# Performance work log

Measured on AMD Instinct MI355X. Metric: run time of the kernel, lower is better.

## Reference

```python
import jax, jax.numpy as jnp
import numpy as np

NUM_EXPERTS = 8
HIDDEN = 1024
INTER = 1024
TOKENS = 2048
TOPK = 2


def setup_inputs() -> dict:
    key = jax.random.key(0)
    ks = jax.random.split(key, 7)
    hidden_states = jax.random.normal(ks[0], (TOKENS, HIDDEN), dtype=jnp.float32)
    router_weights = jax.random.uniform(ks[1], (TOKENS, TOPK), dtype=jnp.float32)
    selected_experts = jax.random.randint(ks[2], (TOKENS, TOPK), 0, NUM_EXPERTS, dtype=jnp.int32)
    token_per_expert = jax.random.randint(ks[3], (NUM_EXPERTS,), 0, 512, dtype=jnp.int32)
    # torch Linear weight layout is [out, in]; chunked along out-dim into E experts.
    # gate/up: [E, INTER, HIDDEN]; down: [E, HIDDEN, INTER]
    scale_h = 1.0 / np.sqrt(HIDDEN)
    scale_i = 1.0 / np.sqrt(INTER)
    gate_w = jax.random.normal(ks[4], (NUM_EXPERTS, INTER, HIDDEN), dtype=jnp.float32) * scale_h
    up_w = jax.random.normal(ks[5], (NUM_EXPERTS, INTER, HIDDEN), dtype=jnp.float32) * scale_h
    down_w = jax.random.normal(ks[6], (NUM_EXPERTS, HIDDEN, INTER), dtype=jnp.float32) * scale_i
    return {
        "hidden_states": hidden_states,
        "router_weights": router_weights,
        "selected_experts": selected_experts,
        "token_per_expert": token_per_expert,
        "gate_w": gate_w,
        "up_w": up_w,
        "down_w": down_w,
    }


def reference(hidden_states, router_weights, selected_experts, token_per_expert, gate_w, up_w, down_w):
    # Math equivalent of permute -> grouped GEMM (gate/up SwiGLU, down) -> unpermute+weighted combine.
    # Each (token, k) pair is routed to expert selected_experts[t,k] and scaled by router_weights[t,k]
    # (cast to fp32 as in the original), then summed over k.
    # Grouped GEMM out = x @ W_e^T; we evaluate every expert densely over all tokens and
    # combine with a one-hot routing matrix (clean, fully vectorized reference).
    x = hidden_states  # [T, H]
    g = jnp.einsum('th,eih->eti', x, gate_w)          # [E, T, I]
    u = jnp.einsum('th,eih->eti', x, up_w)            # [E, T, I]
    h = jax.nn.silu(g) * u                            # [E, T, I]
    out_e = jnp.einsum('eti,ehi->eth', h, down_w)     # [E, T, H]
    # combine[t, e] = sum_k router_weights[t, k] * 1[selected_experts[t, k] == e]
    onehot = jax.nn.one_hot(selected_experts, NUM_EXPERTS, dtype=jnp.float32)  # [T, K, E]
    combine = jnp.einsum('tk,tke->te', router_weights.astype(jnp.float32), onehot)  # [T, E]
    y = jnp.einsum('te,eth->th', combine, out_e)      # [T, H]
    return y
```

## Files before the change

### kernel.cpp

```cpp
#include <hip/hip_runtime.h>

#define T_TOK 2048
#define HID   1024
#define INTER_ 1024
#define NEXP  8
#define NPAIR 4096
#define PERM_MAX 4608

typedef unsigned short u16;
typedef __attribute__((ext_vector_type(8))) short bf16x8;
typedef __attribute__((ext_vector_type(4))) float f32x4;
typedef __attribute__((ext_vector_type(4))) unsigned short us4;
typedef __attribute__((ext_vector_type(4))) unsigned int u32x4;

static __device__ __forceinline__ u16 f2bf(float f) {
  union { float f; unsigned u; } v; v.f = f;
  unsigned u = v.u;
  unsigned r = (u + 0x7fffu + ((u >> 16) & 1u)) >> 16;
  return (u16)r;
}

__global__ __launch_bounds__(256) void k_prep(const float* __restrict__ x,
                                              u16* __restrict__ xb,
                                              float* __restrict__ out) {
  int i = blockIdx.x * 256 + threadIdx.x;
  int base = i * 8;
  f32x4 v0 = *(const f32x4*)(x + base);
  f32x4 v1 = *(const f32x4*)(x + base + 4);
  us4 a = { f2bf(v0[0]), f2bf(v0[1]), f2bf(v0[2]), f2bf(v0[3]) };
  us4 b = { f2bf(v1[0]), f2bf(v1[1]), f2bf(v1[2]), f2bf(v1[3]) };
  *(us4*)(xb + base)     = a;
  *(us4*)(xb + base + 4) = b;
  f32x4 z = {0.f, 0.f, 0.f, 0.f};
  *(f32x4*)(out + base)     = z;
  *(f32x4*)(out + base + 4) = z;
}

__global__ __launch_bounds__(256) void k_route(const int* __restrict__ sel,
                                               int* __restrict__ hdr,
                                               int* __restrict__ perm) {
  __shared__ int cnt[NEXP];
  __shared__ int cur[NEXP];
  int tid = threadIdx.x;
  if (tid < NEXP) cnt[tid] = 0;
  __syncthreads();
  for (int p = tid; p < NPAIR; p += 256) atomicAdd(&cnt[sel[p]], 1);
  __syncthreads();
  if (tid == 0) {
    int acc = 0;
    for (int e = 0; e < NEXP; e++) {
      hdr[e] = acc;
      cur[e] = acc;
      acc += (cnt[e] + 63) & ~63;
    }
    hdr[NEXP] = acc;
  }
  __syncthreads();
  for (int i = tid; i < PERM_MAX; i += 256) perm[i] = -1;
  __syncthreads();
  for (int p = tid; p < NPAIR; p += 256) {
    int e = sel[p];
    int slot = atomicAdd(&cur[e], 1);
    perm[slot] = p;
  }
}

__global__ __launch_bounds__(256) void k_gateup(const u16* __restrict__ xb,
                                                const float* __restrict__ gw,
                                                const float* __restrict__ uw,
                                                const int* __restrict__ hdr,
                                                const int* __restrict__ perm,
                                                u16* __restrict__ hbuf) {
  __shared__ __align__(16) u16 lA[4096];
  __shared__ __align__(16) u16 lBg[4096];
  __shared__ __align__(16) u16 lBu[4096];

  const int tid = threadIdx.x;
  const int lane = tid & 63;
  const int wv = tid >> 6;
  const int n0 = blockIdx.x * 64;
  const int m0 = blockIdx.y * 64;
  const int total = hdr[NEXP];
  if (m0 >= total) return;
  int e = 0;
  #pragma unroll
  for (int k = 1; k < NEXP; k++) if (m0 >= hdr[k]) e = k;

  const int c0 = tid, c1 = 256 + tid;
  const int r0 = c0 >> 3, q0 = c0 & 7;
  const int r1 = c1 >> 3, q1 = c1 & 7;
  const int p0 = perm[m0 + r0]; const int tok0 = (p0 < 0) ? 0 : (p0 >> 1);
  const int p1 = perm[m0 + r1]; const int tok1 = (p1 < 0) ? 0 : (p1 >> 1);
  const u16* gA0 = xb + (size_t)tok0 * HID + q0 * 8;
  const u16* gA1 = xb + (size_t)tok1 * HID + q1 * 8;
  const int lA0 = r0 * 64 + (q0 ^ (r0 & 7)) * 8;
  const int lA1 = r1 * 64 + (q1 ^ (r1 & 7)) * 8;

  const float* gB[4]; const float* gU[4]; int lB[4];
  const size_t ebase = (size_t)e * (size_t)(INTER_ * HID);
  #pragma unroll
  for (int i = 0; i < 4; i++) {
    int c = tid + 256 * i;
    int r = c >> 4, q4 = c & 15;
    gB[i] = gw + ebase + (size_t)(n0 + r) * HID + q4 * 4;
    gU[i] = uw + ebase + (size_t)(n0 + r) * HID + q4 * 4;
    lB[i] = r * 64 + (((q4 >> 1) ^ (r & 7)) * 8) + (q4 & 1) * 4;
  }

  const int wm = wv >> 1, wn = wv & 1;
  const int fr = lane & 15, fq = lane >> 4;

  f32x4 accg[2][2], accu[2][2];
  #pragma unroll
  for (int a = 0; a < 2; a++)
    #pragma unroll
    for (int b = 0; b < 2; b++) {
      accg[a][b] = (f32x4){0.f, 0.f, 0.f, 0.f};
      accu[a][b] = (f32x4){0.f, 0.f, 0.f, 0.f};
    }

  for (int kk = 0; kk < HID / 64; kk++) {
    const int k0 = kk * 64;
    *(u32x4*)&lA[lA0] = *(const u32x4*)(gA0 + k0);
    *(u32x4*)&lA[lA1] = *(const u32x4*)(gA1 + k0);
    #pragma unroll
    for (int i = 0; i < 4; i++) {
      f32x4 vg = *(const f32x4*)(gB[i] + k0);
      f32x4 vu = *(const f32x4*)(gU[i] + k0);
      us4 wg = { f2bf(vg[0]), f2bf(vg[1]), f2bf(vg[2]), f2bf(vg[3]) };
      us4 wu = { f2bf(vu[0]), f2bf(vu[1]), f2bf(vu[2]), f2bf(vu[3]) };
      *(us4*)&lBg[lB[i]] = wg;
      *(us4*)&lBu[lB[i]] = wu;
    }
    __syncthreads();
    #pragma unroll
    for (int kk2 = 0; kk2 < 2; kk2++) {
      bf16x8 af[2], bgf[2], buf_[2];
      #pragma unroll
      for (int m2 = 0; m2 < 2; m2++) {
        int r = wm * 32 + m2 * 16 + fr;
        int q = kk2 * 4 + fq;
        af[m2] = *(const bf16x8*)&lA[r * 64 + (q ^ (r & 7)) * 8];
      }
      #pragma unroll
      for (int n2 = 0; n2 < 2; n2++) {
        int r = wn * 32 + n2 * 16 + fr;
        int q = kk2 * 4 + fq;
        bgf[n2]  = *(const bf16x8*)&lBg[r * 64 + (q ^ (r & 7)) * 8];
        buf_[n2] = *(const bf16x8*)&lBu[r * 64 + (q ^ (r & 7)) * 8];
      }
      #pragma unroll
      for (int m2 = 0; m2 < 2; m2++)
        #pragma unroll
        for (int n2 = 0; n2 < 2; n2++) {
          accg[m2][n2] = __builtin_amdgcn_mfma_f32_16x16x32_bf16(af[m2], bgf[n2],  accg[m2][n2], 0, 0, 0);
          accu[m2][n2] = __builtin_amdgcn_mfma_f32_16x16x32_bf16(af[m2], buf_[n2], accu[m2][n2], 0, 0, 0);
        }
    }
    __syncthreads();
  }

  #pragma unroll
  for (int m2 = 0; m2 < 2; m2++)
    #pragma unroll
    for (int n2 = 0; n2 < 2; n2++)
      #pragma unroll
      for (int q = 0; q < 4; q++) {
        int row = m0 + wm * 32 + m2 * 16 + fq * 4 + q;
        int col = n0 + wn * 32 + n2 * 16 + fr;
        float g = accg[m2][n2][q];
        float u = accu[m2][n2][q];
        float h = (g / (1.0f + __expf(-g))) * u;
        hbuf[(size_t)row * INTER_ + col] = f2bf(h);
      }
}

__global__ __launch_bounds__(256) void k_down(const u16* __restrict__ hbuf,
                                              const float* __restrict__ dw,
                                              const int* __restrict__ hdr,
                                              const int* __restrict__ perm,
                                              const float* __restrict__ rw,
                                              float* __restrict__ out) {
  __shared__ __align__(16) u16 lA[4096];
  __shared__ __align__(16) u16 lB[4096];

  const int tid = threadIdx.x;
  const int lane = tid & 63;
  const int wv = tid >> 6;
  const int n0 = blockIdx.x * 64;
  const int m0 = blockIdx.y * 64;
  const int total = hdr[NEXP];
  if (m0 >= total) return;
  int e = 0;
  #pragma unroll
  for (int k = 1; k < NEXP; k++) if (m0 >= hdr[k]) e = k;

  const int c0 = tid, c1 = 256 + tid;
  const int r0 = c0 >> 3, q0 = c0 & 7;
  const int r1 = c1 >> 3, q1 = c1 & 7;
  const u16* gA0 = hbuf + (size_t)(m0 + r0) * INTER_ + q0 * 8;
  const u16* gA1 = hbuf + (size_t)(m0 + r1) * INTER_ + q1 * 8;
  const int lA0 = r0 * 64 + (q0 ^ (r0 & 7)) * 8;
  const int lA1 = r1 * 64 + (q1 ^ (r1 & 7)) * 8;

  const float* gB[4]; int lBo[4];
  const size_t ebase = (size_t)e * (size_t)(HID * INTER_);
  #pragma unroll
  for (int i = 0; i < 4; i++) {
    int c = tid + 256 * i;
    int r = c >> 4, q4 = c & 15;
    gB[i] = dw + ebase + (size_t)(n0 + r) * INTER_ + q4 * 4;
    lBo[i] = r * 64 + (((q4 >> 1) ^ (r & 7)) * 8) + (q4 & 1) * 4;
  }

  const int wm = wv >> 1, wn = wv & 1;
  const int fr = lane & 15, fq = lane >> 4;

  f32x4 acc[2][2];
  #pragma unroll
  for (int a = 0; a < 2; a++)
    #pragma unroll
    for (int b = 0; b < 2; b++) acc[a][b] = (f32x4){0.f, 0.f, 0.f, 0.f};

  for (int kk = 0; kk < INTER_ / 64; kk++) {
    const int k0 = kk * 64;
    *(u32x4*)&lA[lA0] = *(const u32x4*)(gA0 + k0);
    *(u32x4*)&lA[lA1] = *(const u32x4*)(gA1 + k0);
    #pragma unroll
    for (int i = 0; i < 4; i++) {
      f32x4 vb = *(const f32x4*)(gB[i] + k0);
      us4 wb = { f2bf(vb[0]), f2bf(vb[1]), f2bf(vb[2]), f2bf(vb[3]) };
      *(us4*)&lB[lBo[i]] = wb;
    }
    __syncthreads();
    #pragma unroll
    for (int kk2 = 0; kk2 < 2; kk2++) {
      bf16x8 af[2], bf[2];
      #pragma unroll
      for (int m2 = 0; m2 < 2; m2++) {
        int r = wm * 32 + m2 * 16 + fr;
        int q = kk2 * 4 + fq;
        af[m2] = *(const bf16x8*)&lA[r * 64 + (q ^ (r & 7)) * 8];
      }
      #pragma unroll
      for (int n2 = 0; n2 < 2; n2++) {
        int r = wn * 32 + n2 * 16 + fr;
        int q = kk2 * 4 + fq;
        bf[n2] = *(const bf16x8*)&lB[r * 64 + (q ^ (r & 7)) * 8];
      }
      #pragma unroll
      for (int m2 = 0; m2 < 2; m2++)
        #pragma unroll
        for (int n2 = 0; n2 < 2; n2++)
          acc[m2][n2] = __builtin_amdgcn_mfma_f32_16x16x32_bf16(af[m2], bf[n2], acc[m2][n2], 0, 0, 0);
    }
    __syncthreads();
  }

  #pragma unroll
  for (int m2 = 0; m2 < 2; m2++)
    #pragma unroll
    for (int q = 0; q < 4; q++) {
      int row = m0 + wm * 32 + m2 * 16 + fq * 4 + q;
      int p = perm[row];
      if (p < 0) continue;
      int t = p >> 1;
      float w = rw[p];
      #pragma unroll
      for (int n2 = 0; n2 < 2; n2++) {
        int col = n0 + wn * 32 + n2 * 16 + fr;
        atomicAdd(&out[(size_t)t * HID + col], acc[m2][n2][q] * w);
      }
    }
}

extern "C" void kernel_launch(void* const* d_in, const int* in_sizes, int n_in,
                              void* d_out, int out_size, void* d_ws, size_t ws_size,
                              hipStream_t stream) {
  const float* x   = (const float*)d_in[0];
  const float* rw  = (const float*)d_in[1];
  const int*   sel = (const int*)d_in[2];
  const float* gw  = (const float*)d_in[4];
  const float* uw  = (const float*)d_in[5];
  const float* dw  = (const float*)d_in[6];
  float* out = (float*)d_out;

  char* ws = (char*)d_ws;
  int*  hdr  = (int*)ws;
  int*  perm = (int*)(ws + 1024);
  u16*  xb   = (u16*)(ws + 32768);
  u16*  hbuf = (u16*)(ws + 32768 + 4 * 1024 * 1024);

  k_prep<<<dim3(1024), dim3(256), 0, stream>>>(x, xb, out);
  k_route<<<dim3(1), dim3(256), 0, stream>>>(sel, hdr, perm);
  k_gateup<<<dim3(16, 72), dim3(256), 0, stream>>>(xb, gw, uw, hdr, perm, hbuf);
  k_down<<<dim3(16, 72), dim3(256), 0, stream>>>(hbuf, dw, hdr, perm, rw, out);
}
```

Measured before the change: 101.7 us.

## Pre-convert expert weights to bf16, use direct global-to-LDS loads, 128-row tiles

Adds a separate kernel that converts all gate, up and down weights from fp32 to bf16 once per call. This replaces the per-tile fp32 load and conversion inside each GEMM block, which was repeated by every M-tile. The GEMM kernels now stage A and B tiles with global_load_lds 16-byte transfers and swizzled source addresses. The M tile grows to 128 rows, with expert segments padded to 128, so each weight tile is reused across more tokens. The trade-off is one extra full pass over the 96 MB of fp32 weights plus a bf16 write each call, and more padding rows per expert.

```diff
diff --git a/kernel.cpp b/kernel.cpp
--- a/kernel.cpp
+++ b/kernel.cpp
@@ -1,23 +1,32 @@
 #include <hip/hip_runtime.h>
 
-#define T_TOK 2048
 #define HID   1024
-#define INTER_ 1024
 #define NEXP  8
 #define NPAIR 4096
-#define PERM_MAX 4608
+#define BMPAD 128
+#define PERM_MAX (NPAIR + NEXP * BMPAD)
+#define MT_MAX (PERM_MAX / 128)
 
 typedef unsigned short u16;
 typedef __attribute__((ext_vector_type(8))) short bf16x8;
 typedef __attribute__((ext_vector_type(4))) float f32x4;
 typedef __attribute__((ext_vector_type(4))) unsigned short us4;
-typedef __attribute__((ext_vector_type(4))) unsigned int u32x4;
 
 static __device__ __forceinline__ u16 f2bf(float f) {
   union { float f; unsigned u; } v; v.f = f;
   unsigned u = v.u;
   unsigned r = (u + 0x7fffu + ((u >> 16) & 1u)) >> 16;
   return (u16)r;
+}
+
+static __device__ __forceinline__ void gload16(const void* g, void* l) {
+  __builtin_amdgcn_global_load_lds(
+      (const __attribute__((address_space(1))) unsigned int*)g,
+      (__attribute__((address_space(3))) unsigned int*)l, 16, 0, 0);
+}
+
+static __device__ __forceinline__ f32x4 mfma_bf16(bf16x8 a, bf16x8 b, f32x4 c) {
+  return __builtin_amdgcn_mfma_f32_16x16x32_bf16(a, b, c, 0, 0, 0);
 }
 
 __global__ __launch_bounds__(256) void k_prep(const float* __restrict__ x,
@@ -34,6 +43,27 @@
   f32x4 z = {0.f, 0.f, 0.f, 0.f};
   *(f32x4*)(out + base)     = z;
   *(f32x4*)(out + base + 4) = z;
+}
+
+__global__ __launch_bounds__(256) void k_convw(const float* __restrict__ g,
+                                               const float* __restrict__ u,
+                                               const float* __restrict__ d,
+                                               u16* __restrict__ gb,
+                                               u16* __restrict__ ub,
+                                               u16* __restrict__ db) {
+  const long NTH = 3L << 20;
+  for (long i = (long)blockIdx.x * 256 + threadIdx.x; i < NTH; i += (long)gridDim.x * 256) {
+    int which = (int)(i >> 20);
+    long off = (i & ((1L << 20) - 1)) * 8;
+    const float* src = which == 0 ? g : (which == 1 ? u : d);
+    u16* dst = which == 0 ? gb : (which == 1 ? ub : db);
+    f32x4 v0 = *(const f32x4*)(src + off);
+    f32x4 v1 = *(const f32x4*)(src + off + 4);
+    us4 a = { f2bf(v0[0]), f2bf(v0[1]), f2bf(v0[2]), f2bf(v0[3]) };
+    us4 b = { f2bf(v1[0]), f2bf(v1[1]), f2bf(v1[2]), f2bf(v1[3]) };
+    *(us4*)(dst + off)     = a;
+    *(us4*)(dst + off + 4) = b;
+  }
 }
 
 __global__ __launch_bounds__(256) void k_route(const int* __restrict__ sel,
@@ -51,7 +81,7 @@
     for (int e = 0; e < NEXP; e++) {
       hdr[e] = acc;
       cur[e] = acc;
-      acc += (cnt[e] + 63) & ~63;
+      acc += (cnt[e] + 127) & ~127;
     }
     hdr[NEXP] = acc;
   }
@@ -66,53 +96,50 @@
 }
 
 __global__ __launch_bounds__(256) void k_gateup(const u16* __restrict__ xb,
-                                                const float* __restrict__ gw,
-                                                const float* __restrict__ uw,
+                                                const u16* __restrict__ gwb,
+                                                const u16* __restrict__ uwb,
                                                 const int* __restrict__ hdr,
                                                 const int* __restrict__ perm,
                                                 u16* __restrict__ hbuf) {
-  __shared__ __align__(16) u16 lA[4096];
-  __shared__ __align__(16) u16 lBg[4096];
-  __shared__ __align__(16) u16 lBu[4096];
-
-  const int tid = threadIdx.x;
-  const int lane = tid & 63;
-  const int wv = tid >> 6;
-  const int n0 = blockIdx.x * 64;
-  const int m0 = blockIdx.y * 64;
+  __shared__ __align__(16) u16 lA[128 * 64];
+  __shared__ __align__(16) u16 lBg[64 * 64];
+  __shared__ __align__(16) u16 lBu[64 * 64];
+
+  const int tid = threadIdx.x, lane = tid & 63, wv = tid >> 6;
+  const int n0 = blockIdx.x * 64, m0 = blockIdx.y * 128;
   const int total = hdr[NEXP];
   if (m0 >= total) return;
   int e = 0;
   #pragma unroll
   for (int k = 1; k < NEXP; k++) if (m0 >= hdr[k]) e = k;
 
-  const int c0 = tid, c1 = 256 + tid;
-  const int r0 = c0 >> 3, q0 = c0 & 7;
-  const int r1 = c1 >> 3, q1 = c1 & 7;
-  const int p0 = perm[m0 + r0]; const int tok0 = (p0 < 0) ? 0 : (p0 >> 1);
-  const int p1 = perm[m0 + r1]; const int tok1 = (p1 < 0) ? 0 : (p1 >> 1);
-  const u16* gA0 = xb + (size_t)tok0 * HID + q0 * 8;
-  const u16* gA1 = xb + (size_t)tok1 * HID + q1 * 8;
-  const int lA0 = r0 * 64 + (q0 ^ (r0 & 7)) * 8;
-  const int lA1 = r1 * 64 + (q1 ^ (r1 & 7)) * 8;
-
-  const float* gB[4]; const float* gU[4]; int lB[4];
-  const size_t ebase = (size_t)e * (size_t)(INTER_ * HID);
-  #pragma unroll
-  for (int i = 0; i < 4; i++) {
-    int c = tid + 256 * i;
-    int r = c >> 4, q4 = c & 15;
-    gB[i] = gw + ebase + (size_t)(n0 + r) * HID + q4 * 4;
-    gU[i] = uw + ebase + (size_t)(n0 + r) * HID + q4 * 4;
-    lB[i] = r * 64 + (((q4 >> 1) ^ (r & 7)) * 8) + (q4 & 1) * 4;
+  const u16* srcA[4]; u16* dstA[4];
+  #pragma unroll
+  for (int j = 0; j < 4; j++) {
+    int rt = wv * 32 + j * 8 + (lane >> 3);
+    int p = perm[m0 + rt];
+    int tok = (p < 0) ? 0 : (p >> 1);
+    int sw = (lane & 7) ^ (rt & 7);
+    srcA[j] = xb + (size_t)tok * HID + sw * 8;
+    dstA[j] = &lA[(wv * 32 + j * 8) * 64];
+  }
+  const u16* srcG[2]; const u16* srcU[2]; int dstBo[2];
+  const size_t eb = (size_t)e * (1 << 20);
+  #pragma unroll
+  for (int j = 0; j < 2; j++) {
+    int rt = wv * 16 + j * 8 + (lane >> 3);
+    int sw = (lane & 7) ^ (rt & 7);
+    srcG[j] = gwb + eb + (size_t)(n0 + rt) * HID + sw * 8;
+    srcU[j] = uwb + eb + (size_t)(n0 + rt) * HID + sw * 8;
+    dstBo[j] = (wv * 16 + j * 8) * 64;
   }
 
   const int wm = wv >> 1, wn = wv & 1;
   const int fr = lane & 15, fq = lane >> 4;
 
-  f32x4 accg[2][2], accu[2][2];
-  #pragma unroll
-  for (int a = 0; a < 2; a++)
+  f32x4 accg[4][2], accu[4][2];
+  #pragma unroll
+  for (int a = 0; a < 4; a++)
     #pragma unroll
     for (int b = 0; b < 2; b++) {
       accg[a][b] = (f32x4){0.f, 0.f, 0.f, 0.f};
@@ -121,147 +148,132 @@
 
   for (int kk = 0; kk < HID / 64; kk++) {
     const int k0 = kk * 64;
-    *(u32x4*)&lA[lA0] = *(const u32x4*)(gA0 + k0);
-    *(u32x4*)&lA[lA1] = *(const u32x4*)(gA1 + k0);
-    #pragma unroll
-    for (int i = 0; i < 4; i++) {
-      f32x4 vg = *(const f32x4*)(gB[i] + k0);
-      f32x4 vu = *(const f32x4*)(gU[i] + k0);
-      us4 wg = { f2bf(vg[0]), f2bf(vg[1]), f2bf(vg[2]), f2bf(vg[3]) };
-      us4 wu = { f2bf(vu[0]), f2bf(vu[1]), f2bf(vu[2]), f2bf(vu[3]) };
-      *(us4*)&lBg[lB[i]] = wg;
-      *(us4*)&lBu[lB[i]] = wu;
+    #pragma unroll
+    for (int j = 0; j < 4; j++) gload16(srcA[j] + k0, dstA[j]);
+    #pragma unroll
+    for (int j = 0; j < 2; j++) {
+      gload16(srcG[j] + k0, &lBg[dstBo[j]]);
+      gload16(srcU[j] + k0, &lBu[dstBo[j]]);
     }
     __syncthreads();
     #pragma unroll
     for (int kk2 = 0; kk2 < 2; kk2++) {
-      bf16x8 af[2], bgf[2], buf_[2];
-      #pragma unroll
-      for (int m2 = 0; m2 < 2; m2++) {
-        int r = wm * 32 + m2 * 16 + fr;
-        int q = kk2 * 4 + fq;
+      bf16x8 af[4], bg[2], bu[2];
+      #pragma unroll
+      for (int m2 = 0; m2 < 4; m2++) {
+        int r = wm * 64 + m2 * 16 + fr, q = kk2 * 4 + fq;
         af[m2] = *(const bf16x8*)&lA[r * 64 + (q ^ (r & 7)) * 8];
       }
       #pragma unroll
       for (int n2 = 0; n2 < 2; n2++) {
-        int r = wn * 32 + n2 * 16 + fr;
-        int q = kk2 * 4 + fq;
-        bgf[n2]  = *(const bf16x8*)&lBg[r * 64 + (q ^ (r & 7)) * 8];
-        buf_[n2] = *(const bf16x8*)&lBu[r * 64 + (q ^ (r & 7)) * 8];
-      }
-      #pragma unroll
-      for (int m2 = 0; m2 < 2; m2++)
+        int r = wn * 32 + n2 * 16 + fr, q = kk2 * 4 + fq;
+        bg[n2] = *(const bf16x8*)&lBg[r * 64 + (q ^ (r & 7)) * 8];
+        bu[n2] = *(const bf16x8*)&lBu[r * 64 + (q ^ (r & 7)) * 8];
+      }
+      #pragma unroll
+      for (int m2 = 0; m2 < 4; m2++)
         #pragma unroll
         for (int n2 = 0; n2 < 2; n2++) {
-          accg[m2][n2] = __builtin_amdgcn_mfma_f32_16x16x32_bf16(af[m2], bgf[n2],  accg[m2][n2], 0, 0, 0);
-          accu[m2][n2] = __builtin_amdgcn_mfma_f32_16x16x32_bf16(af[m2], buf_[n2], accu[m2][n2], 0, 0, 0);
+          accg[m2][n2] = mfma_bf16(af[m2], bg[n2], accg[m2][n2]);
+          accu[m2][n2] = mfma_bf16(af[m2], bu[n2], accu[m2][n2]);
         }
     }
     __syncthreads();
   }
 
   #pragma unroll
-  for (int m2 = 0; m2 < 2; m2++)
+  for (int m2 = 0; m2 < 4; m2++)
     #pragma unroll
     for (int n2 = 0; n2 < 2; n2++)
       #pragma unroll
       for (int q = 0; q < 4; q++) {
-        int row = m0 + wm * 32 + m2 * 16 + fq * 4 + q;
+        int row = m0 + wm * 64 + m2 * 16 + fq * 4 + q;
         int col = n0 + wn * 32 + n2 * 16 + fr;
         float g = accg[m2][n2][q];
         float u = accu[m2][n2][q];
         float h = (g / (1.0f + __expf(-g))) * u;
-        hbuf[(size_t)row * INTER_ + col] = f2bf(h);
+        hbuf[(size_t)row * HID + col] = f2bf(h);
       }
 }
 
 __global__ __launch_bounds__(256) void k_down(const u16* __restrict__ hbuf,
-                                              const float* __restrict__ dw,
+                                              const u16* __restrict__ dwb,
                                               const int* __restrict__ hdr,
                                               const int* __restrict__ perm,
                                               const float* __restrict__ rw,
                                               float* __restrict__ out) {
-  __shared__ __align__(16) u16 lA[4096];
-  __shared__ __align__(16) u16 lB[4096];
-
-  const int tid = threadIdx.x;
-  const int lane = tid & 63;
-  const int wv = tid >> 6;
-  const int n0 = blockIdx.x * 64;
-  const int m0 = blockIdx.y * 64;
+  __shared__ __align__(16) u16 lA[128 * 64];
+  __shared__ __align__(16) u16 lB[64 * 64];
+
+  const int tid = threadIdx.x, lane = tid & 63, wv = tid >> 6;
+  const int n0 = blockIdx.x * 64, m0 = blockIdx.y * 128;
   const int total = hdr[NEXP];
   if (m0 >= total) return;
   int e = 0;
   #pragma unroll
   for (int k = 1; k < NEXP; k++) if (m0 >= hdr[k]) e = k;
 
-  const int c0 = tid, c1 = 256 + tid;
-  const int r0 = c0 >> 3, q0 = c0 & 7;
-  const int r1 = c1 >> 3, q1 = c1 & 7;
-  const u16* gA0 = hbuf + (size_t)(m0 + r0) * INTER_ + q0 * 8;
-  const u16* gA1 = hbuf + (size_t)(m0 + r1) * INTER_ + q1 * 8;
-  const int lA0 = r0 * 64 + (q0 ^ (r0 & 7)) * 8;
-  const int lA1 = r1 * 64 + (q1 ^ (r1 & 7)) * 8;
-
-  const float* gB[4]; int lBo[4];
-  const size_t ebase = (size_t)e * (size_t)(HID * INTER_);
-  #pragma unroll
-  for (int i = 0; i < 4; i++) {
-    int c = tid + 256 * i;
-    int r = c >> 4, q4 = c & 15;
-    gB[i] = dw + ebase + (size_t)(n0 + r) * INTER_ + q4 * 4;
-    lBo[i] = r * 64 + (((q4 >> 1) ^ (r & 7)) * 8) + (q4 & 1) * 4;
+  const u16* srcA[4]; u16* dstA[4];
+  #pragma unroll
+  for (int j = 0; j < 4; j++) {
+    int rt = wv * 32 + j * 8 + (lane >> 3);
+    int sw = (lane & 7) ^ (rt & 7);
+    srcA[j] = hbuf + (size_t)(m0 + rt) * HID + sw * 8;
+    dstA[j] = &lA[(wv * 32 + j * 8) * 64];
+  }
+  const u16* srcB[2]; int dstBo[2];
+  const size_t eb = (size_t)e * (1 << 20);
+  #pragma unroll
+  for (int j = 0; j < 2; j++) {
+    int rt = wv * 16 + j * 8 + (lane >> 3);
+    int sw = (lane & 7) ^ (rt & 7);
+    srcB[j] = dwb + eb + (size_t)(n0 + rt) * HID + sw * 8;
+    dstBo[j] = (wv * 16 + j * 8) * 64;
   }
 
   const int wm = wv >> 1, wn = wv & 1;
   const int fr = lane & 15, fq = lane >> 4;
 
-  f32x4 acc[2][2];
-  #pragma unroll
-  for (int a = 0; a < 2; a++)
+  f32x4 acc[4][2];
+  #pragma unroll
+  for (int a = 0; a < 4; a++)
     #pragma unroll
     for (int b = 0; b < 2; b++) acc[a][b] = (f32x4){0.f, 0.f, 0.f, 0.f};
 
-  for (int kk = 0; kk < INTER_ / 64; kk++) {
+  for (int kk = 0; kk < HID / 64; kk++) {
     const int k0 = kk * 64;
-    *(u32x4*)&lA[lA0] = *(const u32x4*)(gA0 + k0);
-    *(u32x4*)&lA[lA1] = *(const u32x4*)(gA1 + k0);
-    #pragma unroll
-    for (int i = 0; i < 4; i++) {
-      f32x4 vb = *(const f32x4*)(gB[i] + k0);
-      us4 wb = { f2bf(vb[0]), f2bf(vb[1]), f2bf(vb[2]), f2bf(vb[3]) };
-      *(us4*)&lB[lBo[i]] = wb;
-    }
+    #pragma unroll
+    for (int j = 0; j < 4; j++) gload16(srcA[j] + k0, dstA[j]);
+    #pragma unroll
+    for (int j = 0; j < 2; j++) gload16(srcB[j] + k0, &lB[dstBo[j]]);
     __syncthreads();
     #pragma unroll
     for (int kk2 = 0; kk2 < 2; kk2++) {
-      bf16x8 af[2], bf[2];
-      #pragma unroll
-      for (int m2 = 0; m2 < 2; m2++) {
-        int r = wm * 32 + m2 * 16 + fr;
-        int q = kk2 * 4 + fq;
+      bf16x8 af[4], bf[2];
+      #pragma unroll
+      for (int m2 = 0; m2 < 4; m2++) {
+        int r = wm * 64 + m2 * 16 + fr, q = kk2 * 4 + fq;
         af[m2] = *(const bf16x8*)&lA[r * 64 + (q ^ (r & 7)) * 8];
       }
       #pragma unroll
       for (int n2 = 0; n2 < 2; n2++) {
-        int r = wn * 32 + n2 * 16 + fr;
-        int q = kk2 * 4 + fq;
+        int r = wn * 32 + n2 * 16 + fr, q = kk2 * 4 + fq;
         bf[n2] = *(const bf16x8*)&lB[r * 64 + (q ^ (r & 7)) * 8];
       }
       #pragma unroll
-      for (int m2 = 0; m2 < 2; m2++)
+      for (int m2 = 0; m2 < 4; m2++)
         #pragma unroll
         for (int n2 = 0; n2 < 2; n2++)
-          acc[m2][n2] = __builtin_amdgcn_mfma_f32_16x16x32_bf16(af[m2], bf[n2], acc[m2][n2], 0, 0, 0);
+          acc[m2][n2] = mfma_bf16(af[m2], bf[n2], acc[m2][n2]);
     }
     __syncthreads();
   }
 
   #pragma unroll
-  for (int m2 = 0; m2 < 2; m2++)
+  for (int m2 = 0; m2 < 4; m2++)
     #pragma unroll
     for (int q = 0; q < 4; q++) {
-      int row = m0 + wm * 32 + m2 * 16 + fq * 4 + q;
+      int row = m0 + wm * 64 + m2 * 16 + fq * 4 + q;
       int p = perm[row];
       if (p < 0) continue;
       int t = p >> 1;
@@ -288,11 +300,15 @@
   char* ws = (char*)d_ws;
   int*  hdr  = (int*)ws;
   int*  perm = (int*)(ws + 1024);
-  u16*  xb   = (u16*)(ws + 32768);
-  u16*  hbuf = (u16*)(ws + 32768 + 4 * 1024 * 1024);
-
-  k_prep<<<dim3(1024), dim3(256), 0, stream>>>(x, xb, out);
-  k_route<<<dim3(1), dim3(256), 0, stream>>>(sel, hdr, perm);
-  k_gateup<<<dim3(16, 72), dim3(256), 0, stream>>>(xb, gw, uw, hdr, perm, hbuf);
-  k_down<<<dim3(16, 72), dim3(256), 0, stream>>>(hbuf, dw, hdr, perm, rw, out);
-}
+  u16*  xb   = (u16*)(ws + (1 << 16));
+  u16*  gwb  = xb + (2 << 20);
+  u16*  uwb  = gwb + (8 << 20);
+  u16*  dwb  = uwb + (8 << 20);
+  u16*  hbuf = dwb + (8 << 20);
+
+  k_prep <<<dim3(1024), dim3(256), 0, stream>>>(x, xb, out);
+  k_convw<<<dim3(4096), dim3(256), 0, stream>>>(gw, uw, dw, gwb, uwb, dwb);
+  k_route<<<dim3(1),    dim3(256), 0, stream>>>(sel, hdr, perm);
+  k_gateup<<<dim3(16, MT_MAX), dim3(256), 0, stream>>>(xb, gwb, uwb, hdr, perm, hbuf);
+  k_down  <<<dim3(16, MT_MAX), dim3(256), 0, stream>>>(hbuf, dwb, hdr, perm, rw, out);
+}
```

Result: slower. 114.4 us (+12.5%).
